# Kernel optimization log

Hardware: AMD Instinct MI355X
Metric: run time of the kernel (lower is better)

Reference implementation:

```python
import jax, jax.numpy as jnp
import numpy as np

HEADS = 8
DIM_HEAD = 64
SCALE = DIM_HEAD ** -0.5


def setup_inputs() -> dict:
    key = jax.random.key(0)
    k1, k2, k3 = jax.random.split(key, 3)
    b, p, n, dim = 2, 16, 512, 512
    inner = HEADS * DIM_HEAD  # 512
    x = jax.random.normal(k1, (b, p, n, dim), dtype=jnp.float32)
    W_qkv = jax.random.normal(k2, (dim, 3 * inner), dtype=jnp.float32) * (dim ** -0.5)
    W_out = jax.random.normal(k3, (inner, dim), dtype=jnp.float32) * (inner ** -0.5)
    b_out = jnp.zeros((dim,), dtype=jnp.float32)
    return {"x": x, "W_qkv": W_qkv, "W_out": W_out, "b_out": b_out}


def reference(x, W_qkv, W_out, b_out):
    b, p, n, dim = x.shape
    # QKV projection (no bias), split into q, k, v
    qkv = jnp.einsum('bpnd,de->bpne', x, W_qkv)
    q, k, v = jnp.split(qkv, 3, axis=-1)
    # (b, p, n, h*d) -> (b, p, h, n, d)
    def to_heads(t):
        return t.reshape(b, p, n, HEADS, DIM_HEAD).transpose(0, 1, 3, 2, 4)
    q, k, v = to_heads(q), to_heads(k), to_heads(v)
    # attention scores: (b, p, h, n, n)
    dots = jnp.einsum('bphnd,bphmd->bphnm', q, k) * SCALE
    attn = jax.nn.softmax(dots, axis=-1)
    out = jnp.einsum('bphnm,bphmd->bphnd', attn, v)
    # (b, p, h, n, d) -> (b, p, n, h*d)
    out = out.transpose(0, 1, 3, 2, 4).reshape(b, p, n, HEADS * DIM_HEAD)
    # output projection (dropout rate = 0.0 -> identity)
    return jnp.einsum('bpne,ed->bpnd', out, W_out) + b_out
```

## Files before the change

### kernel.cpp

```cpp
#include <hip/hip_runtime.h>
#include <hip/hip_bf16.h>

typedef short bf16x8 __attribute__((ext_vector_type(8)));
typedef short bf16x4 __attribute__((ext_vector_type(4)));
typedef float f32x4  __attribute__((ext_vector_type(4)));

__device__ __forceinline__ unsigned short f2bf(float f) {
    union { float fv; unsigned int u; } v; v.fv = f;
    unsigned int r = v.u + 0x7FFFu + ((v.u >> 16) & 1u);
    return (unsigned short)(r >> 16);
}

__device__ __forceinline__ void gload16(const short* g, short* l) {
    __builtin_amdgcn_global_load_lds(
        (const __attribute__((address_space(1))) void*)g,
        (__attribute__((address_space(3))) void*)l, 16, 0, 0);
}

__global__ __launch_bounds__(256) void cvt_x(
    const float* __restrict__ x, short* __restrict__ xb)
{
    size_t i = ((size_t)blockIdx.x * 256 + threadIdx.x) * 8;
    f32x4 a = *(const f32x4*)(x + i);
    f32x4 b = *(const f32x4*)(x + i + 4);
    bf16x8 s;
    #pragma unroll
    for (int e = 0; e < 4; ++e) { s[e] = (short)f2bf(a[e]); s[4 + e] = (short)f2bf(b[e]); }
    *(bf16x8*)(xb + i) = s;
}

__global__ __launch_bounds__(256) void prep_w(
    const float* __restrict__ Wqkv, const float* __restrict__ Wout,
    short* __restrict__ Wqkvt, short* __restrict__ Woutt)
{
    int idx = blockIdx.x * 256 + threadIdx.x;
    int n = idx >> 9, k = idx & 511;
    Wqkvt[idx] = (short)f2bf(Wqkv[(size_t)k * 1536 + n]);
    if (idx < 512 * 512) {
        Woutt[idx] = (short)f2bf(Wout[(size_t)k * 512 + n]);
    }
}

template<int F32OUT>
__global__ __launch_bounds__(256, 2) void gemm_db(
    const short* __restrict__ A, const short* __restrict__ Bt,
    short* __restrict__ Cb, float* __restrict__ Cf, const float* __restrict__ bias,
    int M, int N, int K, int NB)
{
    __shared__ short lds[2][2][128 * 64];
    const int t    = threadIdx.x;
    const int lane = t & 63;
    const int wid  = t >> 6;
    const int l15  = lane & 15;
    const int lg   = lane >> 4;

    const int cpx = gridDim.x >> 3;
    const int swz = (blockIdx.x & 7) * cpx + (blockIdx.x >> 3);
    const int m0 = (swz / NB) * 128;
    const int n0 = (swz % NB) * 128;

    const int wm = (wid >> 1) * 64;
    const int wn = (wid & 1) * 64;

    const int scol = 8 * ((lane & 7) ^ ((lane >> 3) & 7));

    float bval[4];
    if constexpr (F32OUT) {
        #pragma unroll
        for (int ni = 0; ni < 4; ++ni) bval[ni] = bias[n0 + wn + ni * 16 + l15];
    }

    f32x4 acc[4][4];
    #pragma unroll
    for (int i = 0; i < 4; ++i)
        #pragma unroll
        for (int j = 0; j < 4; ++j)
            acc[i][j] = f32x4{0.f, 0.f, 0.f, 0.f};

    const int NT = K >> 6;

    auto stage = [&](int buf, int tk) {
        #pragma unroll
        for (int j = 0; j < 4; ++j) {
            const int r = wid * 32 + j * 8 + (lane >> 3);
            gload16(A  + (size_t)(m0 + r) * K + tk * 64 + scol,
                    &lds[buf][0][(wid * 32 + j * 8) * 64]);
            gload16(Bt + (size_t)(n0 + r) * K + tk * 64 + scol,
                    &lds[buf][1][(wid * 32 + j * 8) * 64]);
        }
    };

    stage(0, 0);

    for (int tk = 0; tk < NT; ++tk) {
        const int cur = tk & 1;
        if (tk + 1 < NT) {
            stage(cur ^ 1, tk + 1);
            asm volatile("s_waitcnt vmcnt(8)" ::: "memory");
        } else {
            asm volatile("s_waitcnt vmcnt(0)" ::: "memory");
        }
        __builtin_amdgcn_s_barrier();

        bf16x8 af[4][2], bg[4][2];
        #pragma unroll
        for (int kk = 0; kk < 2; ++kk) {
            #pragma unroll
            for (int mi = 0; mi < 4; ++mi)
                af[mi][kk] = *(const bf16x8*)&lds[cur][0][
                    (wm + mi * 16 + l15) * 64 + (((kk * 4 + lg) ^ (l15 & 7)) * 8)];
            #pragma unroll
            for (int ni = 0; ni < 4; ++ni)
                bg[ni][kk] = *(const bf16x8*)&lds[cur][1][
                    (wn + ni * 16 + l15) * 64 + (((kk * 4 + lg) ^ (l15 & 7)) * 8)];
        }

        __builtin_amdgcn_s_setprio(1);
        #pragma unroll
        for (int kk = 0; kk < 2; ++kk)
            #pragma unroll
            for (int mi = 0; mi < 4; ++mi)
                #pragma unroll
                for (int ni = 0; ni < 4; ++ni)
                    acc[mi][ni] = __builtin_amdgcn_mfma_f32_16x16x32_bf16(
                        af[mi][kk], bg[ni][kk], acc[mi][ni], 0, 0, 0);
        __builtin_amdgcn_s_setprio(0);
        __builtin_amdgcn_s_barrier();
    }

    #pragma unroll
    for (int mi = 0; mi < 4; ++mi) {
        #pragma unroll
        for (int ni = 0; ni < 4; ++ni) {
            const int col = n0 + wn + ni * 16 + l15;
            #pragma unroll
            for (int r = 0; r < 4; ++r) {
                const int rowi = m0 + wm + mi * 16 + 4 * lg + r;
                if constexpr (F32OUT) {
                    Cf[(size_t)rowi * N + col] = acc[mi][ni][r] + bval[ni];
                } else {
                    Cb[(size_t)rowi * N + col] = (short)f2bf(acc[mi][ni][r]);
                }
            }
        }
    }
}

__global__ __launch_bounds__(512, 4) void attn_kernel(
    const short* __restrict__ qkv, short* __restrict__ attn_out)
{
    __shared__ short Kl[2][64][72];
    __shared__ short Vt[2][64][76];
    const int t    = threadIdx.x;
    const int lane = t & 63;
    const int wid  = t >> 6;
    const int l15  = lane & 15;
    const int lg   = lane >> 4;
    const int pairid = blockIdx.x & 255;
    const int qh  = blockIdx.x >> 8;
    const int bp  = pairid >> 3;
    const int h   = pairid & 7;
    const size_t tok0 = (size_t)bp * 512;
    const int q0   = qh * 256 + wid * 32;
    const int qcol = h * 64;

    bf16x8 qf[2][2];
    #pragma unroll
    for (int mj = 0; mj < 2; ++mj)
        #pragma unroll
        for (int kf = 0; kf < 2; ++kf)
            qf[mj][kf] = *(const bf16x8*)(qkv + (tok0 + q0 + mj * 16 + l15) * 1536
                                          + qcol + kf * 32 + 8 * lg);

    f32x4 ot[4][2];
    #pragma unroll
    for (int i = 0; i < 4; ++i)
        #pragma unroll
        for (int j = 0; j < 2; ++j)
            ot[i][j] = f32x4{0.f, 0.f, 0.f, 0.f};
    float mrun[2] = {-1e30f, -1e30f}, lrun[2] = {0.f, 0.f};

    const int sn = t >> 3;
    const int sd = (t & 7) * 8;

    const short* kvbase = qkv + (tok0 + sn) * 1536 + qcol + sd;
    bf16x8 kreg = *(const bf16x8*)(kvbase + 512);
    bf16x8 vreg = *(const bf16x8*)(kvbase + 1024);

    const float C = 0.18033688011112042f;

    for (int tkv = 0; tkv < 8; ++tkv) {
        const int cur = tkv & 1;
        *(bf16x8*)&Kl[cur][sn][sd] = kreg;
        #pragma unroll
        for (int i = 0; i < 8; ++i) Vt[cur][sd + i][sn] = vreg[i];
        if (tkv < 7) {
            const short* nxt = kvbase + (size_t)(tkv + 1) * 64 * 1536;
            kreg = *(const bf16x8*)(nxt + 512);
            vreg = *(const bf16x8*)(nxt + 1024);
        }
        __syncthreads();

        f32x4 st[4][2];
        #pragma unroll
        for (int i = 0; i < 4; ++i)
            #pragma unroll
            for (int j = 0; j < 2; ++j)
                st[i][j] = f32x4{0.f, 0.f, 0.f, 0.f};
        #pragma unroll
        for (int kf = 0; kf < 2; ++kf) {
            #pragma unroll
            for (int ni = 0; ni < 4; ++ni) {
                bf16x8 kfr = *(const bf16x8*)&Kl[cur][ni * 16 + l15][kf * 32 + 8 * lg];
                #pragma unroll
                for (int mj = 0; mj < 2; ++mj)
                    st[ni][mj] = __builtin_amdgcn_mfma_f32_16x16x32_bf16(
                        kfr, qf[mj][kf], st[ni][mj], 0, 0, 0);
            }
        }

        #pragma unroll
        for (int mj = 0; mj < 2; ++mj) {
            float pm = -1e30f;
            #pragma unroll
            for (int ni = 0; ni < 4; ++ni)
                #pragma unroll
                for (int r = 0; r < 4; ++r) {
                    st[ni][mj][r] *= C;
                    pm = fmaxf(pm, st[ni][mj][r]);
                }
            pm = fmaxf(pm, __shfl_xor(pm, 16));
            pm = fmaxf(pm, __shfl_xor(pm, 32));
            if (!__all(pm <= mrun[mj] + 8.f)) {
                const float mnew = fmaxf(mrun[mj], pm);
                const float fsc  = __builtin_amdgcn_exp2f(mrun[mj] - mnew);
                lrun[mj] *= fsc;
                #pragma unroll
                for (int di = 0; di < 4; ++di)
                    ot[di][mj] *= fsc;
                mrun[mj] = mnew;
            }
            float ps = 0.f;
            #pragma unroll
            for (int ni = 0; ni < 4; ++ni)
                #pragma unroll
                for (int r = 0; r < 4; ++r) {
                    float e = __builtin_amdgcn_exp2f(st[ni][mj][r] - mrun[mj]);
                    st[ni][mj][r] = e;
                    ps += e;
                }
            ps += __shfl_xor(ps, 16);
            ps += __shfl_xor(ps, 32);
            lrun[mj] += ps;
        }

        #pragma unroll
        for (int ni = 0; ni < 4; ++ni) {
            bf16x4 pb[2];
            #pragma unroll
            for (int mj = 0; mj < 2; ++mj)
                #pragma unroll
                for (int r = 0; r < 4; ++r)
                    pb[mj][r] = (short)f2bf(st[ni][mj][r]);
            #pragma unroll
            for (int di = 0; di < 4; ++di) {
                bf16x4 av = *(const bf16x4*)&Vt[cur][di * 16 + l15][ni * 16 + 4 * lg];
                #pragma unroll
                for (int mj = 0; mj < 2; ++mj)
                    ot[di][mj] = __builtin_amdgcn_mfma_f32_16x16x16bf16_1k(
                        av, pb[mj], ot[di][mj], 0, 0, 0);
            }
        }
    }

    float inv[2];
    #pragma unroll
    for (int mj = 0; mj < 2; ++mj) inv[mj] = 1.f / lrun[mj];
    #pragma unroll
    for (int di = 0; di < 4; ++di)
        #pragma unroll
        for (int mj = 0; mj < 2; ++mj) {
            const size_t tok = tok0 + q0 + mj * 16 + l15;
            const int col = qcol + di * 16 + 4 * lg;
            bf16x4 o4;
            #pragma unroll
            for (int r = 0; r < 4; ++r)
                o4[r] = (short)f2bf(ot[di][mj][r] * inv[mj]);
            *(bf16x4*)(attn_out + tok * 512 + col) = o4;
        }
}

extern "C" void kernel_launch(void* const* d_in, const int* in_sizes, int n_in,
                              void* d_out, int out_size, void* d_ws, size_t ws_size,
                              hipStream_t stream) {
    const float* x    = (const float*)d_in[0];
    const float* Wqkv = (const float*)d_in[1];
    const float* Wout = (const float*)d_in[2];
    const float* bout = (const float*)d_in[3];
    float* out = (float*)d_out;

    char* ws = (char*)d_ws;
    short* qkvb  = (short*)(ws);
    short* xb    = (short*)(ws + 50331648ull);
    short* attnb = xb;
    short* Wqkvt = (short*)(ws + 67108864ull);
    short* Woutt = (short*)(ws + 68681728ull);

    cvt_x<<<4096, 256, 0, stream>>>(x, xb);
    prep_w<<<3072, 256, 0, stream>>>(Wqkv, Wout, Wqkvt, Woutt);

    gemm_db<0><<<1536, 256, 0, stream>>>(xb, Wqkvt, qkvb, nullptr, nullptr,
                                         16384, 1536, 512, 12);

    attn_kernel<<<512, 512, 0, stream>>>(qkvb, attnb);

    gemm_db<1><<<512, 256, 0, stream>>>(attnb, Woutt, nullptr, out, bout,
                                        16384, 512, 512, 4);
}
```

Measured before the change: 103.3 us.

## Swizzle attention K/V LDS, async-load K, tile weight transpose, fold softmax scale

The per-element weight transpose is replaced with a shared-memory tiled transpose so both reads and writes are coalesced. In the attention kernel, K tiles are loaded straight into LDS with global_load_lds into an XOR-swizzled layout, and V is stored transposed into a swizzled padded layout to reduce bank conflicts. The barrier now comes before the next prefetch, and wave priority is raised around the MFMA blocks. The softmax scale is folded into an FMA inside the exponent instead of a separate multiply, and the hand-written bf16 rounding is swapped for the intrinsic conversion. These changes touch several parts at once, and the swizzle index maths is easy to get wrong.

```diff
diff --git a/kernel.cpp b/kernel.cpp
--- a/kernel.cpp
+++ b/kernel.cpp
@@ -9,6 +9,12 @@
     union { float fv; unsigned int u; } v; v.fv = f;
     unsigned int r = v.u + 0x7FFFu + ((v.u >> 16) & 1u);
     return (unsigned short)(r >> 16);
+}
+
+__device__ __forceinline__ short f2bf_n(float f) {
+    union { __hip_bfloat16 h; short s; } u;
+    u.h = __float2bfloat16(f);
+    return u.s;
 }
 
 __device__ __forceinline__ void gload16(const short* g, short* l) {
@@ -29,16 +35,29 @@
     *(bf16x8*)(xb + i) = s;
 }
 
-__global__ __launch_bounds__(256) void prep_w(
+__global__ __launch_bounds__(256) void tr_w2(
     const float* __restrict__ Wqkv, const float* __restrict__ Wout,
     short* __restrict__ Wqkvt, short* __restrict__ Woutt)
 {
-    int idx = blockIdx.x * 256 + threadIdx.x;
-    int n = idx >> 9, k = idx & 511;
-    Wqkvt[idx] = (short)f2bf(Wqkv[(size_t)k * 1536 + n]);
-    if (idx < 512 * 512) {
-        Woutt[idx] = (short)f2bf(Wout[(size_t)k * 512 + n]);
-    }
+    __shared__ float tile[32][33];
+    const int b = blockIdx.x;
+    const float* src; short* dst; int N, bb;
+    if (b < 768) { src = Wqkv; dst = Wqkvt; N = 1536; bb = b; }
+    else         { src = Wout; dst = Woutt; N = 512;  bb = b - 768; }
+    const int tx = threadIdx.x;
+    const int nb = N >> 5;
+    const int k0 = (bb / nb) * 32;
+    const int n0 = (bb % nb) * 32;
+    const int r  = tx >> 3;
+    const int c4 = (tx & 7) * 4;
+    f32x4 v = *(const f32x4*)(src + (size_t)(k0 + r) * N + n0 + c4);
+    #pragma unroll
+    for (int e = 0; e < 4; ++e) tile[r][c4 + e] = v[e];
+    __syncthreads();
+    bf16x4 o;
+    #pragma unroll
+    for (int e = 0; e < 4; ++e) o[e] = (short)f2bf(tile[c4 + e][r]);
+    *(bf16x4*)(dst + (size_t)(n0 + r) * 512 + k0 + c4) = o;
 }
 
 template<int F32OUT>
@@ -149,8 +168,8 @@
 __global__ __launch_bounds__(512, 4) void attn_kernel(
     const short* __restrict__ qkv, short* __restrict__ attn_out)
 {
-    __shared__ short Kl[2][64][72];
-    __shared__ short Vt[2][64][76];
+    __shared__ short Kl[2][4096];
+    __shared__ short Vt[2][5120];
     const int t    = threadIdx.x;
     const int lane = t & 63;
     const int wid  = t >> 6;
@@ -180,26 +199,29 @@
             ot[i][j] = f32x4{0.f, 0.f, 0.f, 0.f};
     float mrun[2] = {-1e30f, -1e30f}, lrun[2] = {0.f, 0.f};
 
+    const int krow = t >> 3;
+    const short* Ksrc0 = qkv + (tok0 + krow) * 1536 + 512 + qcol
+                         + 8 * ((t & 7) ^ (krow & 7));
     const int sn = t >> 3;
     const int sd = (t & 7) * 8;
-
-    const short* kvbase = qkv + (tok0 + sn) * 1536 + qcol + sd;
-    bf16x8 kreg = *(const bf16x8*)(kvbase + 512);
-    bf16x8 vreg = *(const bf16x8*)(kvbase + 1024);
+    const short* Vsrc0 = qkv + (tok0 + sn) * 1536 + 1024 + qcol + sd;
+    const int kvp = (sn & 7) | (((sn >> 3) ^ (t & 7)) << 3);
+
+    gload16(Ksrc0, &Kl[0][t * 8]);
+    bf16x8 vreg = *(const bf16x8*)(Vsrc0);
 
     const float C = 0.18033688011112042f;
 
     for (int tkv = 0; tkv < 8; ++tkv) {
         const int cur = tkv & 1;
-        *(bf16x8*)&Kl[cur][sn][sd] = kreg;
-        #pragma unroll
-        for (int i = 0; i < 8; ++i) Vt[cur][sd + i][sn] = vreg[i];
+        #pragma unroll
+        for (int i = 0; i < 8; ++i)
+            Vt[cur][(sd + i) * 80 + kvp] = vreg[i];
+        __syncthreads();
         if (tkv < 7) {
-            const short* nxt = kvbase + (size_t)(tkv + 1) * 64 * 1536;
-            kreg = *(const bf16x8*)(nxt + 512);
-            vreg = *(const bf16x8*)(nxt + 1024);
-        }
-        __syncthreads();
+            gload16(Ksrc0 + (size_t)(tkv + 1) * 64 * 1536, &Kl[cur ^ 1][t * 8]);
+            vreg = *(const bf16x8*)(Vsrc0 + (size_t)(tkv + 1) * 64 * 1536);
+        }
 
         f32x4 st[4][2];
         #pragma unroll
@@ -207,17 +229,20 @@
             #pragma unroll
             for (int j = 0; j < 2; ++j)
                 st[i][j] = f32x4{0.f, 0.f, 0.f, 0.f};
+        __builtin_amdgcn_s_setprio(1);
         #pragma unroll
         for (int kf = 0; kf < 2; ++kf) {
             #pragma unroll
             for (int ni = 0; ni < 4; ++ni) {
-                bf16x8 kfr = *(const bf16x8*)&Kl[cur][ni * 16 + l15][kf * 32 + 8 * lg];
+                bf16x8 kfr = *(const bf16x8*)&Kl[cur][
+                    (ni * 16 + l15) * 64 + (((kf * 4 + lg) ^ (l15 & 7)) * 8)];
                 #pragma unroll
                 for (int mj = 0; mj < 2; ++mj)
                     st[ni][mj] = __builtin_amdgcn_mfma_f32_16x16x32_bf16(
                         kfr, qf[mj][kf], st[ni][mj], 0, 0, 0);
             }
         }
+        __builtin_amdgcn_s_setprio(0);
 
         #pragma unroll
         for (int mj = 0; mj < 2; ++mj) {
@@ -225,19 +250,17 @@
             #pragma unroll
             for (int ni = 0; ni < 4; ++ni)
                 #pragma unroll
-                for (int r = 0; r < 4; ++r) {
-                    st[ni][mj][r] *= C;
+                for (int r = 0; r < 4; ++r)
                     pm = fmaxf(pm, st[ni][mj][r]);
-                }
             pm = fmaxf(pm, __shfl_xor(pm, 16));
             pm = fmaxf(pm, __shfl_xor(pm, 32));
+            pm *= C;
             if (!__all(pm <= mrun[mj] + 8.f)) {
                 const float mnew = fmaxf(mrun[mj], pm);
                 const float fsc  = __builtin_amdgcn_exp2f(mrun[mj] - mnew);
                 lrun[mj] *= fsc;
                 #pragma unroll
-                for (int di = 0; di < 4; ++di)
-                    ot[di][mj] *= fsc;
+                for (int di = 0; di < 4; ++di) ot[di][mj] *= fsc;
                 mrun[mj] = mnew;
             }
             float ps = 0.f;
@@ -245,7 +268,8 @@
             for (int ni = 0; ni < 4; ++ni)
                 #pragma unroll
                 for (int r = 0; r < 4; ++r) {
-                    float e = __builtin_amdgcn_exp2f(st[ni][mj][r] - mrun[mj]);
+                    float e = __builtin_amdgcn_exp2f(
+                        __builtin_fmaf(st[ni][mj][r], C, -mrun[mj]));
                     st[ni][mj][r] = e;
                     ps += e;
                 }
@@ -254,6 +278,7 @@
             lrun[mj] += ps;
         }
 
+        __builtin_amdgcn_s_setprio(1);
         #pragma unroll
         for (int ni = 0; ni < 4; ++ni) {
             bf16x4 pb[2];
@@ -261,16 +286,21 @@
             for (int mj = 0; mj < 2; ++mj)
                 #pragma unroll
                 for (int r = 0; r < 4; ++r)
-                    pb[mj][r] = (short)f2bf(st[ni][mj][r]);
+                    pb[mj][r] = f2bf_n(st[ni][mj][r]);
             #pragma unroll
             for (int di = 0; di < 4; ++di) {
-                bf16x4 av = *(const bf16x4*)&Vt[cur][di * 16 + l15][ni * 16 + 4 * lg];
+                const int row = di * 16 + l15;
+                bf16x4 av = *(const bf16x4*)&Vt[cur][
+                    row * 80
+                    + (((2 * ni + (lg >> 1)) ^ (2 * di + (l15 >> 3))) * 8)
+                    + 4 * (lg & 1)];
                 #pragma unroll
                 for (int mj = 0; mj < 2; ++mj)
                     ot[di][mj] = __builtin_amdgcn_mfma_f32_16x16x16bf16_1k(
                         av, pb[mj], ot[di][mj], 0, 0, 0);
             }
         }
+        __builtin_amdgcn_s_setprio(0);
     }
 
     float inv[2];
@@ -285,7 +315,7 @@
             bf16x4 o4;
             #pragma unroll
             for (int r = 0; r < 4; ++r)
-                o4[r] = (short)f2bf(ot[di][mj][r] * inv[mj]);
+                o4[r] = f2bf_n(ot[di][mj][r] * inv[mj]);
             *(bf16x4*)(attn_out + tok * 512 + col) = o4;
         }
 }
@@ -307,7 +337,7 @@
     short* Woutt = (short*)(ws + 68681728ull);
 
     cvt_x<<<4096, 256, 0, stream>>>(x, xb);
-    prep_w<<<3072, 256, 0, stream>>>(Wqkv, Wout, Wqkvt, Woutt);
+    tr_w2<<<1024, 256, 0, stream>>>(Wqkv, Wout, Wqkvt, Woutt);
 
     gemm_db<0><<<1536, 256, 0, stream>>>(xb, Wqkvt, qkvb, nullptr, nullptr,
                                          16384, 1536, 512, 12);
```

Result: faster. 97.98 us (-5.2%).
